# Kernel tuning notes

Hardware: AMD Instinct MI355X
Metric: run time of the kernel (lower is better)

Reference implementation:

```python
import jax, jax.numpy as jnp
import numpy as np

B, S, D, V, K = 256, 2048, 64, 10000, 5


def setup_inputs() -> dict:
    key = jax.random.key(0)
    k1, k2, k3 = jax.random.split(key, 3)
    # right-padded ragged sequences: first L[i] entries are nonzero POI ids, rest 0
    lengths = jax.random.randint(k1, (B,), K + 1, S + 1)
    vals = jax.random.randint(k2, (B, S), 1, V)
    pos = jnp.arange(S)
    seqs = jnp.where(pos[None, :] < lengths[:, None], vals, 0)
    seq_embeddings = jax.random.normal(k3, (B, S, D), dtype=jnp.float32)
    return {"seqs": seqs, "seq_embeddings": seq_embeddings, "k": K}


def reference(seqs, seq_embeddings, k):
    # NOTE: pywt.wavedec('db1') followed by pywt.waverec('db1') truncated to the
    # original length is an exact perfect-reconstruction round trip, so the
    # original fft_prob equals binary_seq; the math reduces to:
    #   binary match vs anchor -> L1 normalize -> zero last (j+1) -> roll(j+1)
    # and roll of a zeroed tail over length L == shift-right by j+1, zero front.
    Bsz, Slen = seqs.shape
    valid = seqs != 0                      # [B,S] (right-padded)
    L = valid.sum(axis=1)                  # [B] true lengths
    pos = jnp.arange(Slen)[None, :]        # [1,S]
    in_range = pos < L[:, None]            # [B,S]

    avg = jnp.zeros((Bsz, Slen), dtype=jnp.float32)
    for j in range(k):
        # anchor index: real_poi[-(j+1)], frozen at 0 once j+1 >= L
        anchor = jnp.maximum(L - 1 - j, 0)                       # [B]
        aval = jnp.take_along_axis(seqs, anchor[:, None], axis=1)  # [B,1]
        binary = ((seqs == aval) & in_range).astype(jnp.float32)   # [B,S]
        prob = binary / binary.sum(axis=1, keepdims=True)
        # zero last j+1 of valid region, then roll by j+1 within length L
        # == shift-right by j+1 with zero fill, masked to t < L
        shifted = jnp.pad(prob, ((0, 0), (j + 1, 0)))[:, :Slen]
        shifted = jnp.where(in_range, shifted, 0.0)
        avg = avg + shifted
    avg = avg / k                                                 # mean over k probs

    # masked weighted pooling over the sequence dim
    return jnp.einsum('bs,bsd->bd', avg, seq_embeddings)
```

## Files before the change

kernel.cpp:

```cpp
#include <hip/hip_runtime.h>

#define BATCH 256
#define SLEN  2048
#define DDIM  64
#define MAXK  8

__global__ __launch_bounds__(256) void wave_kernel(
    const int*   __restrict__ seqs,
    const float* __restrict__ emb,
    const int*   __restrict__ kptr,
    float*       __restrict__ out)
{
    __shared__ int   sseq[SLEN];
    __shared__ float avg[SLEN];
    __shared__ int   sL;
    __shared__ int   anchors[MAXK];
    __shared__ int   counts[MAXK];
    __shared__ float winv[MAXK];
    __shared__ float partial[4][DDIM];

    const int b    = blockIdx.x;
    const int tid  = threadIdx.x;
    const int lane = tid & 63;
    const int wave = tid >> 6;
    const int k    = kptr[0];

    if (tid == 0) sL = 0;
    if (tid < MAXK) counts[tid] = 0;
    for (int s = tid; s < SLEN; s += 256) avg[s] = 0.0f;
    __syncthreads();

    int cnt = 0;
    for (int s = tid; s < SLEN; s += 256) {
        int v = seqs[b * SLEN + s];
        sseq[s] = v;
        cnt += (v != 0);
    }
    #pragma unroll
    for (int off = 32; off; off >>= 1) cnt += __shfl_down(cnt, off, 64);
    if (lane == 0) atomicAdd(&sL, cnt);
    __syncthreads();

    const int L = sL;

    if (tid < k) {
        int a = L - 1 - tid;
        if (a < 0) a = 0;
        anchors[tid] = sseq[a];
    }
    __syncthreads();

    int aj[MAXK];
    #pragma unroll
    for (int j = 0; j < MAXK; ++j)
        aj[j] = (j < k) ? anchors[j] : -1;

    int lc[MAXK];
    #pragma unroll
    for (int j = 0; j < MAXK; ++j) lc[j] = 0;
    for (int s = tid; s < L; s += 256) {
        int v = sseq[s];
        #pragma unroll
        for (int j = 0; j < MAXK; ++j)
            if (v == aj[j]) lc[j]++;
    }
    #pragma unroll
    for (int j = 0; j < MAXK; ++j)
        if (j < k && lc[j]) atomicAdd(&counts[j], lc[j]);
    __syncthreads();

    if (tid < k) winv[tid] = 1.0f / ((float)k * (float)counts[tid]);
    __syncthreads();

    float wj[MAXK];
    #pragma unroll
    for (int j = 0; j < MAXK; ++j)
        wj[j] = (j < k) ? winv[j] : 0.0f;

    for (int s = tid; s < L; s += 256) {
        int v = sseq[s];
        #pragma unroll
        for (int j = 0; j < MAXK; ++j) {
            if (v == aj[j]) {
                int r = s + j + 1;
                if (r < L) atomicAdd(&avg[r], wj[j]);
            }
        }
    }
    __syncthreads();

    float acc = 0.0f;
    const float* embb = emb + (size_t)b * SLEN * DDIM;
    for (int sb = wave * 512; sb < (wave + 1) * 512; sb += 64) {
        float wv = avg[sb + lane];
        unsigned long long m = __ballot(wv != 0.0f);
        while (m) {
            int i = __ffsll((long long)m) - 1;
            m &= (m - 1);
            float wgt = avg[sb + i];
            acc += wgt * embb[(sb + i) * DDIM + lane];
        }
    }
    partial[wave][lane] = acc;
    __syncthreads();

    if (wave == 0) {
        float o = partial[0][lane] + partial[1][lane]
                + partial[2][lane] + partial[3][lane];
        out[b * DDIM + lane] = o;
    }
}

extern "C" void kernel_launch(void* const* d_in, const int* in_sizes, int n_in,
                              void* d_out, int out_size, void* d_ws, size_t ws_size,
                              hipStream_t stream) {
    const int*   seqs = (const int*)d_in[0];
    const float* emb  = (const float*)d_in[1];
    const int*   kptr = (const int*)d_in[2];
    float*       out  = (float*)d_out;

    wave_kernel<<<BATCH, 256, 0, stream>>>(seqs, emb, kptr, out);
}
```

Measured before the change: 167.9 us.

## Replace shared avg buffer with event list and single-wave gather

Instead of scattering weights into a shared avg array and scanning it with ballots, each thread records (position, anchor index) events into a shared list while counting matches. After one barrier, a single wave walks the event list and gathers embedding rows, computing each weight from the final counts. Sequence loads become vectorized int4 reads, and the kernel needs fewer barriers. The gather is serialized onto one wave and events beyond the list capacity would be dropped. Duplicate positions now cause repeated row loads instead of one combined weight.

```diff
diff --git a/kernel.cpp b/kernel.cpp
--- a/kernel.cpp
+++ b/kernel.cpp
@@ -4,6 +4,7 @@
 #define SLEN  2048
 #define DDIM  64
 #define MAXK  8
+#define EVCAP 2048
 
 __global__ __launch_bounds__(256) void wave_kernel(
     const int*   __restrict__ seqs,
@@ -11,13 +12,11 @@
     const int*   __restrict__ kptr,
     float*       __restrict__ out)
 {
-    __shared__ int   sseq[SLEN];
-    __shared__ float avg[SLEN];
-    __shared__ int   sL;
-    __shared__ int   anchors[MAXK];
-    __shared__ int   counts[MAXK];
-    __shared__ float winv[MAXK];
-    __shared__ float partial[4][DDIM];
+    __shared__ int sseq[SLEN];
+    __shared__ int wcnt[4];
+    __shared__ int counts[MAXK];
+    __shared__ int nev;
+    __shared__ int ev[EVCAP];
 
     const int b    = blockIdx.x;
     const int tid  = threadIdx.x;
@@ -25,89 +24,69 @@
     const int wave = tid >> 6;
     const int k    = kptr[0];
 
-    if (tid == 0) sL = 0;
+    if (tid == 0) nev = 0;
     if (tid < MAXK) counts[tid] = 0;
-    for (int s = tid; s < SLEN; s += 256) avg[s] = 0.0f;
+
+    const int4* sp = (const int4*)(seqs + (size_t)b * SLEN);
+    int4 a0 = sp[2 * tid];
+    int4 a1 = sp[2 * tid + 1];
+    ((int4*)sseq)[2 * tid]     = a0;
+    ((int4*)sseq)[2 * tid + 1] = a1;
+
+    int vr[8] = {a0.x, a0.y, a0.z, a0.w, a1.x, a1.y, a1.z, a1.w};
+    int cnt = 0;
+    #pragma unroll
+    for (int i = 0; i < 8; ++i) cnt += (vr[i] != 0);
+    #pragma unroll
+    for (int off = 32; off; off >>= 1) cnt += __shfl_down(cnt, off, 64);
+    if (lane == 0) wcnt[wave] = cnt;
+
     __syncthreads();
 
-    int cnt = 0;
-    for (int s = tid; s < SLEN; s += 256) {
-        int v = seqs[b * SLEN + s];
-        sseq[s] = v;
-        cnt += (v != 0);
-    }
-    #pragma unroll
-    for (int off = 32; off; off >>= 1) cnt += __shfl_down(cnt, off, 64);
-    if (lane == 0) atomicAdd(&sL, cnt);
-    __syncthreads();
-
-    const int L = sL;
-
-    if (tid < k) {
-        int a = L - 1 - tid;
-        if (a < 0) a = 0;
-        anchors[tid] = sseq[a];
-    }
-    __syncthreads();
+    const int L = wcnt[0] + wcnt[1] + wcnt[2] + wcnt[3];
 
     int aj[MAXK];
     #pragma unroll
-    for (int j = 0; j < MAXK; ++j)
-        aj[j] = (j < k) ? anchors[j] : -1;
+    for (int j = 0; j < MAXK; ++j) {
+        int a = L - 1 - j;
+        if (a < 0) a = 0;
+        aj[j] = (j < k) ? sseq[a] : 0;
+    }
 
-    int lc[MAXK];
+    const int sbase = tid * 8;
     #pragma unroll
-    for (int j = 0; j < MAXK; ++j) lc[j] = 0;
-    for (int s = tid; s < L; s += 256) {
-        int v = sseq[s];
-        #pragma unroll
-        for (int j = 0; j < MAXK; ++j)
-            if (v == aj[j]) lc[j]++;
-    }
-    #pragma unroll
-    for (int j = 0; j < MAXK; ++j)
-        if (j < k && lc[j]) atomicAdd(&counts[j], lc[j]);
-    __syncthreads();
-
-    if (tid < k) winv[tid] = 1.0f / ((float)k * (float)counts[tid]);
-    __syncthreads();
-
-    float wj[MAXK];
-    #pragma unroll
-    for (int j = 0; j < MAXK; ++j)
-        wj[j] = (j < k) ? winv[j] : 0.0f;
-
-    for (int s = tid; s < L; s += 256) {
-        int v = sseq[s];
-        #pragma unroll
-        for (int j = 0; j < MAXK; ++j) {
-            if (v == aj[j]) {
-                int r = s + j + 1;
-                if (r < L) atomicAdd(&avg[r], wj[j]);
+    for (int i = 0; i < 8; ++i) {
+        int v = vr[i];
+        if (v != 0) {
+            #pragma unroll
+            for (int j = 0; j < MAXK; ++j) {
+                if (v == aj[j]) {
+                    atomicAdd(&counts[j], 1);
+                    int r = sbase + i + j + 1;
+                    if (r < L) {
+                        int e = atomicAdd(&nev, 1);
+                        if (e < EVCAP) ev[e] = r | (j << 16);
+                    }
+                }
             }
         }
     }
-    __syncthreads();
 
-    float acc = 0.0f;
-    const float* embb = emb + (size_t)b * SLEN * DDIM;
-    for (int sb = wave * 512; sb < (wave + 1) * 512; sb += 64) {
-        float wv = avg[sb + lane];
-        unsigned long long m = __ballot(wv != 0.0f);
-        while (m) {
-            int i = __ffsll((long long)m) - 1;
-            m &= (m - 1);
-            float wgt = avg[sb + i];
-            acc += wgt * embb[(sb + i) * DDIM + lane];
-        }
-    }
-    partial[wave][lane] = acc;
     __syncthreads();
 
     if (wave == 0) {
-        float o = partial[0][lane] + partial[1][lane]
-                + partial[2][lane] + partial[3][lane];
-        out[b * DDIM + lane] = o;
+        int n = nev;
+        if (n > EVCAP) n = EVCAP;
+        float acc = 0.0f;
+        const float* embb = emb + (size_t)b * SLEN * DDIM;
+        for (int e = 0; e < n; ++e) {
+            int p = ev[e];
+            int r = p & 0xFFFF;
+            int j = p >> 16;
+            float w = 1.0f / ((float)k * (float)counts[j]);
+            acc += w * embb[r * DDIM + lane];
+        }
+        out[b * DDIM + lane] = acc;
     }
 }
 
```

Result: faster. 164.1 us (-2.3%).
